# Optimization experiments

Measured on AMD Instinct MI355X. Metric: run time of the kernel, lower is better.

The kernel has to match this reference:

```python
import jax, jax.numpy as jnp
import numpy as np

B = 8192   # batch of independent theta draws (ABM calibration ensemble)
T = 4096   # recurrence length (__init__ T)
THETA_DIM = 11  # beta, g1..g4, b1..b4, sigma, r


def setup_inputs() -> dict:
    key = jax.random.key(0)
    k1, k2 = jax.random.split(key)
    # uniform[0,1) guarantees beta>0, sigma>0, r>=0 as asserted in the module
    theta = jax.random.uniform(k1, (B, THETA_DIM), dtype=jnp.float32)
    epsilons = jax.random.normal(k2, (B, T), dtype=jnp.float32)
    return {"theta": theta, "epsilons": epsilons}


def reference(theta, epsilons):
    # Brock-Hommes recurrence (Eqs. 39-40 of arXiv:2202.00625), vmapped over batch.
    beta = theta[:, 0]        # [B]
    g = theta[:, 1:5]         # [B,4]
    b = theta[:, 5:9]         # [B,4]
    sigma = theta[:, 9]       # [B]
    r = theta[:, 10]          # [B]
    R = 1.0 + r               # [B]

    def step(carry, eps_t):
        x1, x2, x3 = carry    # x[t-1], x[t-2], x[t-3], each [B]
        Rx2 = R * x2
        # exponent: [B,4]
        exponent = (beta * (x1 - Rx2))[:, None] * (g * x3[:, None] + b - Rx2[:, None])
        w = jax.nn.softmax(exponent, axis=-1)                 # [B,4]
        mean = jnp.sum(w * (g * x1[:, None] + b), axis=-1)    # [B]
        x_t = (mean + eps_t * sigma) / R                      # [B]
        return (x_t, x1, x2), x_t

    z = jnp.zeros(theta.shape[0], dtype=theta.dtype)
    # initial carry of zeros matches x[-1]=x[-2]=x[-3]=0 in the torch code
    _, xs = jax.lax.scan(step, (z, z, z), epsilons.T)  # xs: [T,B]
    return xs.T  # [B,T]
```

## Files before the change

### kernel.cpp

```cpp
#include <hip/hip_runtime.h>

#define THETA_DIM 11
#define BQ   16
#define TILE 64
#define OPAD 68

__device__ __forceinline__ float qdpp_b1(float v) {
  return __builtin_bit_cast(float,
      __builtin_amdgcn_update_dpp(0, __builtin_bit_cast(int, v), 0xB1, 0xF, 0xF, true));
}
__device__ __forceinline__ float qdpp_4e(float v) {
  return __builtin_bit_cast(float,
      __builtin_amdgcn_update_dpp(0, __builtin_bit_cast(int, v), 0x4E, 0xF, 0xF, true));
}
__device__ __forceinline__ float quad_max(float v) {
  v = fmaxf(v, qdpp_b1(v)); v = fmaxf(v, qdpp_4e(v)); return v;
}
__device__ __forceinline__ float quad_min(float v) {
  v = fminf(v, qdpp_b1(v)); v = fminf(v, qdpp_4e(v)); return v;
}
__device__ __forceinline__ float quad_sum(float v) {
  v = v + qdpp_b1(v); v = v + qdpp_4e(v); return v;
}

__device__ __forceinline__ float bh_step(
    float es, float& x1, float& x2,
    float& c1, float& dqM, float& dqm, float& cc,
    float bl2e, float bl2eR, float negR, float g, float bb,
    float gR, float bR) {
  const float A  = fmaf(bl2e, x1, -c1);
  const float dq = (A >= 0.0f) ? dqM : dqm;
  const float t  = A * dq;
  const float p  = __builtin_amdgcn_exp2f(t);
  const float pc = p * cc;
  const float num = quad_sum(pc);
  const float den = quad_sum(p);
  const float x  = fmaf(num, __builtin_amdgcn_rcpf(den), es);
  const float qn  = fmaf(negR, x1, fmaf(g, x2, bb));
  const float c1n = bl2eR * x1;
  const float qmaxn = quad_max(qn);
  const float qminn = quad_min(qn);
  dqM = qn - qmaxn;
  dqm = qn - qminn;
  c1  = c1n;
  x2  = x1; x1 = x;
  cc  = fmaf(gR, x, bR);
  return x;
}

__global__ void __launch_bounds__(64, 1)
bh_kernel(const float* __restrict__ theta, const float* __restrict__ eps,
          float* __restrict__ out, int Tn) {
  __shared__ float out_s[BQ][OPAD];

  const int lane = threadIdx.x;
  const int c  = lane >> 2;
  const int j  = lane & 3;
  const int cb = blockIdx.x * BQ;
  const int b  = cb + c;

  const float* th = theta + b * THETA_DIM;
  const float beta = th[0];
  const float g    = th[1 + j];
  const float bb   = th[5 + j];
  const float sig  = th[9];
  const float r    = th[10];
  const float R    = 1.0f + r;
  const float invR = 1.0f / R;
  const float L2E  = 1.4426950408889634f;
  const float bl2e  = beta * L2E;
  const float bl2eR = bl2e * R;
  const float negR  = -R;
  const float gR = g * invR;
  const float bR = bb * invR;
  const float sR = sig * invR;

  float x1 = 0.f, x2 = 0.f;
  float c1 = 0.f;
  float q0 = bb;
  float qmax0 = quad_max(q0), qmin0 = quad_min(q0);
  float dqM = q0 - qmax0, dqm = q0 - qmin0;
  float cc = bR;

  const float* ep = eps + (size_t)b * Tn;
  const int tlast = Tn - 4;
  float4 eA = *(const float4*)(ep + 0);
  float4 eB = *(const float4*)(ep + 4);

  const int col  = lane & 15;
  const int rsub = lane >> 4;

  const bool j0 = (j == 0), j1 = (j == 1), j2 = (j == 2);

  int t = 0;
  const int NT = Tn / TILE;
  for (int tile = 0; tile < NT; ++tile) {
    float* oc = &out_s[c][0];

    #pragma unroll 4
    for (int g4 = 0; g4 < TILE / 4; ++g4) {
      const float4 ecur = eA;
      eA = eB;
      int tn = t + 8; tn = (tn > tlast) ? tlast : tn;
      eB = *(const float4*)(ep + tn);
      const float es0 = ecur.x * sR, es1 = ecur.y * sR;
      const float es2 = ecur.z * sR, es3 = ecur.w * sR;

      const float xw0 = bh_step(es0, x1,x2, c1,dqM,dqm,cc, bl2e,bl2eR,negR,g,bb,gR,bR);
      const float xw1 = bh_step(es1, x1,x2, c1,dqM,dqm,cc, bl2e,bl2eR,negR,g,bb,gR,bR);
      const float xw2 = bh_step(es2, x1,x2, c1,dqM,dqm,cc, bl2e,bl2eR,negR,g,bb,gR,bR);
      const float xw3 = bh_step(es3, x1,x2, c1,dqM,dqm,cc, bl2e,bl2eR,negR,g,bb,gR,bR);

      const float xw = j0 ? xw0 : (j1 ? xw1 : (j2 ? xw2 : xw3));
      oc[g4 * 4 + j] = xw;
      t += 4;
    }

    const int t0 = tile * TILE;
    #pragma unroll
    for (int i = 0; i < 4; ++i) {
      const float4 o4 = *(const float4*)&out_s[i*4 + rsub][col*4];
      *(float4*)(out + (size_t)(cb + i*4 + rsub) * Tn + t0 + col*4) = o4;
    }
  }
}

extern "C" void kernel_launch(void* const* d_in, const int* in_sizes, int n_in,
                              void* d_out, int out_size, void* d_ws, size_t ws_size,
                              hipStream_t stream) {
  const float* theta = (const float*)d_in[0];
  const float* eps   = (const float*)d_in[1];
  float* out = (float*)d_out;
  const int B  = in_sizes[0] / THETA_DIM;
  const int Tn = in_sizes[1] / B;
  const int blocks = B / BQ;
  bh_kernel<<<blocks, 64, 0, stream>>>(theta, eps, out, Tn);
}
```

Baseline: 542.0 us.

## Map one batch element per lane with packed-float softmax instead of quad DPP

Each thread now handles a whole batch element, evaluating the four softmax terms with packed two-wide float ops instead of spreading them across four lanes with DPP reductions. This removes cross-lane shuffle latency from the serial recurrence chain. Epsilon prefetch becomes a three-stage register pipeline of 16 values, and outputs are written directly per thread without shared-memory staging. The trade-off is a quarter as many waves (128 blocks), leaving many CUs idle, and more serial work per lane.

Result: faster. 491.4 us (-9.3%).

```diff
diff --git a/kernel.cpp b/kernel.cpp
--- a/kernel.cpp
+++ b/kernel.cpp
@@ -1,127 +1,101 @@
 #include <hip/hip_runtime.h>
 
 #define THETA_DIM 11
-#define BQ   16
-#define TILE 64
-#define OPAD 68
 
-__device__ __forceinline__ float qdpp_b1(float v) {
-  return __builtin_bit_cast(float,
-      __builtin_amdgcn_update_dpp(0, __builtin_bit_cast(int, v), 0xB1, 0xF, 0xF, true));
-}
-__device__ __forceinline__ float qdpp_4e(float v) {
-  return __builtin_bit_cast(float,
-      __builtin_amdgcn_update_dpp(0, __builtin_bit_cast(int, v), 0x4E, 0xF, 0xF, true));
-}
-__device__ __forceinline__ float quad_max(float v) {
-  v = fmaxf(v, qdpp_b1(v)); v = fmaxf(v, qdpp_4e(v)); return v;
-}
-__device__ __forceinline__ float quad_min(float v) {
-  v = fminf(v, qdpp_b1(v)); v = fminf(v, qdpp_4e(v)); return v;
-}
-__device__ __forceinline__ float quad_sum(float v) {
-  v = v + qdpp_b1(v); v = v + qdpp_4e(v); return v;
-}
+typedef float v2f __attribute__((ext_vector_type(2)));
 
-__device__ __forceinline__ float bh_step(
-    float es, float& x1, float& x2,
-    float& c1, float& dqM, float& dqm, float& cc,
-    float bl2e, float bl2eR, float negR, float g, float bb,
-    float gR, float bR) {
-  const float A  = fmaf(bl2e, x1, -c1);
-  const float dq = (A >= 0.0f) ? dqM : dqm;
-  const float t  = A * dq;
-  const float p  = __builtin_amdgcn_exp2f(t);
-  const float pc = p * cc;
-  const float num = quad_sum(pc);
-  const float den = quad_sum(p);
-  const float x  = fmaf(num, __builtin_amdgcn_rcpf(den), es);
-  const float qn  = fmaf(negR, x1, fmaf(g, x2, bb));
-  const float c1n = bl2eR * x1;
-  const float qmaxn = quad_max(qn);
-  const float qminn = quad_min(qn);
-  dqM = qn - qmaxn;
-  dqm = qn - qminn;
-  c1  = c1n;
-  x2  = x1; x1 = x;
-  cc  = fmaf(gR, x, bR);
-  return x;
-}
+__device__ __forceinline__ v2f v2(float s) { return (v2f){s, s}; }
 
 __global__ void __launch_bounds__(64, 1)
 bh_kernel(const float* __restrict__ theta, const float* __restrict__ eps,
           float* __restrict__ out, int Tn) {
-  __shared__ float out_s[BQ][OPAD];
+  const int b = blockIdx.x * 64 + threadIdx.x;
 
-  const int lane = threadIdx.x;
-  const int c  = lane >> 2;
-  const int j  = lane & 3;
-  const int cb = blockIdx.x * BQ;
-  const int b  = cb + c;
-
-  const float* th = theta + b * THETA_DIM;
+  const float* th = theta + (size_t)b * THETA_DIM;
   const float beta = th[0];
-  const float g    = th[1 + j];
-  const float bb   = th[5 + j];
-  const float sig  = th[9];
-  const float r    = th[10];
-  const float R    = 1.0f + r;
+  const v2f g01 = {th[1], th[2]}, g23 = {th[3], th[4]};
+  const v2f b01 = {th[5], th[6]}, b23 = {th[7], th[8]};
+  const float sig = th[9];
+  const float R   = 1.0f + th[10];
   const float invR = 1.0f / R;
   const float L2E  = 1.4426950408889634f;
   const float bl2e  = beta * L2E;
   const float bl2eR = bl2e * R;
-  const float negR  = -R;
-  const float gR = g * invR;
-  const float bR = bb * invR;
-  const float sR = sig * invR;
+  const float sR    = sig * invR;
+  const v2f gR01 = g01 * v2(invR), gR23 = g23 * v2(invR);
+  const v2f bR01 = b01 * v2(invR), bR23 = b23 * v2(invR);
+  const v2f nR   = v2(-R);
 
   float x1 = 0.f, x2 = 0.f;
-  float c1 = 0.f;
-  float q0 = bb;
-  float qmax0 = quad_max(q0), qmin0 = quad_min(q0);
-  float dqM = q0 - qmax0, dqm = q0 - qmin0;
-  float cc = bR;
+  float m1 = 0.f;
+  v2f q01 = b01, q23 = b23;
+  v2f c01 = bR01, c23 = bR23;
+  v2f qmm;
+  {
+    v2f mx = __builtin_elementwise_max(q01, q23);
+    v2f mn = __builtin_elementwise_min(q01, q23);
+    qmm = (v2f){fmaxf(mx.x, mx.y), fminf(mn.x, mn.y)};
+  }
+
+  auto step = [&](float e) -> float {
+    const float A  = fmaf(bl2e, x1, -m1);
+    const v2f  uv  = v2(A) * qmm;
+    const float m  = fmaxf(uv.x, uv.y);
+    const v2f  e01 = __builtin_elementwise_fma(v2(A), q01, v2(-m));
+    const v2f  e23 = __builtin_elementwise_fma(v2(A), q23, v2(-m));
+    const v2f  p01 = {__builtin_amdgcn_exp2f(e01.x), __builtin_amdgcn_exp2f(e01.y)};
+    const v2f  p23 = {__builtin_amdgcn_exp2f(e23.x), __builtin_amdgcn_exp2f(e23.y)};
+    const v2f  w01  = __builtin_elementwise_fma(g01, v2(x2), b01);
+    const v2f  w23  = __builtin_elementwise_fma(g23, v2(x2), b23);
+    const v2f  q01n = __builtin_elementwise_fma(nR, v2(x1), w01);
+    const v2f  q23n = __builtin_elementwise_fma(nR, v2(x1), w23);
+    const v2f  mxv  = __builtin_elementwise_max(q01n, q23n);
+    const v2f  mnv  = __builtin_elementwise_min(q01n, q23n);
+    const float m1n = bl2eR * x1;
+    const v2f  nv  = __builtin_elementwise_fma(p23, c23, p01 * c01);
+    const float num = nv.x + nv.y;
+    const v2f  dv  = p01 + p23;
+    const float den = dv.x + dv.y;
+    const float x  = fmaf(num, __builtin_amdgcn_rcpf(den), e * sR);
+    x2 = x1; x1 = x;
+    m1 = m1n; q01 = q01n; q23 = q23n;
+    qmm = (v2f){fmaxf(mxv.x, mxv.y), fminf(mnv.x, mnv.y)};
+    c01 = __builtin_elementwise_fma(gR01, v2(x), bR01);
+    c23 = __builtin_elementwise_fma(gR23, v2(x), bR23);
+    return x;
+  };
 
   const float* ep = eps + (size_t)b * Tn;
-  const int tlast = Tn - 4;
-  float4 eA = *(const float4*)(ep + 0);
-  float4 eB = *(const float4*)(ep + 4);
+  float* op = out + (size_t)b * Tn;
 
-  const int col  = lane & 15;
-  const int rsub = lane >> 4;
+  float4 cA[4], cB[4], cC[4];
+  #pragma unroll
+  for (int i = 0; i < 4; ++i) cA[i] = *(const float4*)(ep + i * 4);
+  #pragma unroll
+  for (int i = 0; i < 4; ++i) cB[i] = *(const float4*)(ep + 16 + i * 4);
 
-  const bool j0 = (j == 0), j1 = (j == 1), j2 = (j == 2);
+  const int NB = Tn / 16;
+  int t0 = 0;
+  for (int blk = 0; blk < NB; ++blk) {
+    int tl = t0 + 32;
+    if (tl > Tn - 16) tl = Tn - 16;
+    const float* lp = ep + tl;
+    #pragma unroll
+    for (int i = 0; i < 4; ++i) cC[i] = *(const float4*)(lp + i * 4);
 
-  int t = 0;
-  const int NT = Tn / TILE;
-  for (int tile = 0; tile < NT; ++tile) {
-    float* oc = &out_s[c][0];
-
-    #pragma unroll 4
-    for (int g4 = 0; g4 < TILE / 4; ++g4) {
-      const float4 ecur = eA;
-      eA = eB;
-      int tn = t + 8; tn = (tn > tlast) ? tlast : tn;
-      eB = *(const float4*)(ep + tn);
-      const float es0 = ecur.x * sR, es1 = ecur.y * sR;
-      const float es2 = ecur.z * sR, es3 = ecur.w * sR;
-
-      const float xw0 = bh_step(es0, x1,x2, c1,dqM,dqm,cc, bl2e,bl2eR,negR,g,bb,gR,bR);
-      const float xw1 = bh_step(es1, x1,x2, c1,dqM,dqm,cc, bl2e,bl2eR,negR,g,bb,gR,bR);
-      const float xw2 = bh_step(es2, x1,x2, c1,dqM,dqm,cc, bl2e,bl2eR,negR,g,bb,gR,bR);
-      const float xw3 = bh_step(es3, x1,x2, c1,dqM,dqm,cc, bl2e,bl2eR,negR,g,bb,gR,bR);
-
-      const float xw = j0 ? xw0 : (j1 ? xw1 : (j2 ? xw2 : xw3));
-      oc[g4 * 4 + j] = xw;
-      t += 4;
+    #pragma unroll
+    for (int i = 0; i < 4; ++i) {
+      float4 o;
+      o.x = step(cA[i].x);
+      o.y = step(cA[i].y);
+      o.z = step(cA[i].z);
+      o.w = step(cA[i].w);
+      *(float4*)(op + t0 + i * 4) = o;
     }
 
-    const int t0 = tile * TILE;
     #pragma unroll
-    for (int i = 0; i < 4; ++i) {
-      const float4 o4 = *(const float4*)&out_s[i*4 + rsub][col*4];
-      *(float4*)(out + (size_t)(cb + i*4 + rsub) * Tn + t0 + col*4) = o4;
-    }
+    for (int i = 0; i < 4; ++i) { cA[i] = cB[i]; cB[i] = cC[i]; }
+    t0 += 16;
   }
 }
 
@@ -133,6 +107,6 @@
   float* out = (float*)d_out;
   const int B  = in_sizes[0] / THETA_DIM;
   const int Tn = in_sizes[1] / B;
-  const int blocks = B / BQ;
+  const int blocks = B / 64;
   bh_kernel<<<blocks, 64, 0, stream>>>(theta, eps, out, Tn);
 }
```
